# Performance work log

Hardware: AMD Instinct MI355X
Metric: run time of the kernel (lower is better)

## Reference

```python
import jax, jax.numpy as jnp
import numpy as np

B, T, C, H = 4, 2048, 1024, 16
D = C // H  # head dim = 64


def setup_inputs() -> dict:
    key = jax.random.key(0)
    k_x, k_wa, k_ba, k_wp, k_bp = jax.random.split(key, 5)
    s = 1.0 / np.sqrt(C)
    return {
        "x": jax.random.normal(k_x, (B, T, C), dtype=jnp.float32),
        "w_attn": jax.random.uniform(k_wa, (C, 3 * C), minval=-s, maxval=s, dtype=jnp.float32),
        "b_attn": jax.random.uniform(k_ba, (3 * C,), minval=-s, maxval=s, dtype=jnp.float32),
        "w_proj": jax.random.uniform(k_wp, (C, C), minval=-s, maxval=s, dtype=jnp.float32),
        "b_proj": jax.random.uniform(k_bp, (C,), minval=-s, maxval=s, dtype=jnp.float32),
    }


def reference(x, w_attn, b_attn, w_proj, b_proj):
    b, t, c = x.shape
    qkv = x @ w_attn + b_attn  # [b, t, 3c]
    q, k, v = jnp.split(qkv, 3, axis=-1)
    # [b, h, t, d]
    q = q.reshape(b, t, H, D).transpose(0, 2, 1, 3)
    k = k.reshape(b, t, H, D).transpose(0, 2, 1, 3)
    v = v.reshape(b, t, H, D).transpose(0, 2, 1, 3)
    scale = 1.0 / np.sqrt(D)
    logits = jnp.einsum("bhqd,bhkd->bhqk", q, k) * scale
    causal = jnp.tril(jnp.ones((t, t), dtype=bool))
    logits = jnp.where(causal, logits, jnp.finfo(logits.dtype).min)
    attn = jax.nn.softmax(logits, axis=-1)
    y = jnp.einsum("bhqk,bhkd->bhqd", attn, v)
    y = y.transpose(0, 2, 1, 3).reshape(b, t, c)
    return y @ w_proj + b_proj
```

## Files before the change

### kernel.cpp

```cpp
#include <hip/hip_runtime.h>


using u16 = unsigned short;
using u32 = unsigned int;
using bf16x8 = __attribute__((ext_vector_type(8))) __bf16;
using f32x4  = __attribute__((ext_vector_type(4))) float;
using f32x16 = __attribute__((ext_vector_type(16))) float;
using u16x8  = __attribute__((ext_vector_type(8))) u16;
using u16x4  = __attribute__((ext_vector_type(4))) u16;
using u32x2  = __attribute__((ext_vector_type(2))) u32;
using u32x4  = __attribute__((ext_vector_type(4))) u32;
using fvec4  = __attribute__((ext_vector_type(4))) float;

__device__ __forceinline__ u16 f2bf(float f) {
  u32 u = __builtin_bit_cast(u32, f);
  u32 r = (u + 0x7FFFu + ((u >> 16) & 1u)) >> 16;
  return (u16)r;
}

__device__ __forceinline__ u32 cvtpk(float lo, float hi) {
  u32 r;
  asm("v_cvt_pk_bf16_f32 %0, %1, %2" : "=v"(r) : "v"(lo), "v"(hi));
  return r;
}

__device__ __forceinline__ f32x4 mfma16(bf16x8 a, bf16x8 b, f32x4 c) {
  return __builtin_amdgcn_mfma_f32_16x16x32_bf16(a, b, c, 0, 0, 0);
}

__device__ __forceinline__ f32x16 mfma32(bf16x8 a, bf16x8 b, f32x16 c) {
  return __builtin_amdgcn_mfma_f32_32x32x16_bf16(a, b, c, 0, 0, 0);
}

__device__ __forceinline__ void gld16(const u16* g, u16* l) {
  __builtin_amdgcn_global_load_lds(
      (const __attribute__((address_space(1))) void*)g,
      (__attribute__((address_space(3))) void*)l, 16, 0, 0);
}

__global__ __launch_bounds__(256) void conv_kernel(
    const float* __restrict__ in, u16* __restrict__ out) {
  const size_t i = ((size_t)blockIdx.x * 256 + threadIdx.x) * 8;
  fvec4 a = *(const fvec4*)(in + i);
  fvec4 b = *(const fvec4*)(in + i + 4);
  u16x8 h;
#pragma unroll
  for (int j = 0; j < 4; ++j) { h[j] = f2bf(a[j]); h[4 + j] = f2bf(b[j]); }
  *(u16x8*)(out + i) = h;
}

__global__ __launch_bounds__(256) void transpose_conv_kernel(
    const float* __restrict__ W, u16* __restrict__ Wt, int K, int N) {
  __shared__ float tile[32][33];
  const int n0 = blockIdx.x * 32, k0 = blockIdx.y * 32;
  const int tx = threadIdx.x, ty = threadIdx.y;
#pragma unroll
  for (int j = 0; j < 4; ++j)
    tile[ty + j * 8][tx] = W[(size_t)(k0 + ty + j * 8) * N + n0 + tx];
  __syncthreads();
#pragma unroll
  for (int j = 0; j < 4; ++j)
    Wt[(size_t)(n0 + ty + j * 8) * K + k0 + tx] = f2bf(tile[tx][ty + j * 8]);
}

template <bool QKV>
__global__ __launch_bounds__(256) void gemm_kernel(
    const u16* __restrict__ A, const u16* __restrict__ Bt,
    const float* __restrict__ bias, void* __restrict__ Cp,
    u16* __restrict__ vt, int M, int N, int K) {
  constexpr float SC = 0.18033688011112042f;
  __shared__ u16 As[2][4096];
  __shared__ u16 Bs[2][4096];
  const int tid = threadIdx.x;
  const int l = tid & 63, w = tid >> 6;
  const int l15 = l & 15, l16 = l >> 4;
  const int wm = (w >> 1) * 64, wn = (w & 1) * 64;

  const u32 nwg = gridDim.x * gridDim.y;
  u32 f = blockIdx.y * gridDim.x + blockIdx.x;
  f = (f & 7) * (nwg >> 3) + (f >> 3);
  const long mbase = (long)(f / gridDim.x) * 128;
  const long nbase = (long)(f % gridDim.x) * 128;

  const int srow = tid >> 2;
  const int scol = ((tid & 3) ^ ((srow >> 1) & 3)) * 8;
  const u16* gA0 = A + (mbase + srow) * (long)K + scol;
  const u16* gA1 = gA0 + 64 * (long)K;
  const u16* gB0 = Bt + (nbase + srow) * (long)K + scol;
  const u16* gB1 = gB0 + 64 * (long)K;

  f32x4 acc[4][4] = {};
  const int NT = K >> 5;

#define STAGE(buf, koff)                         \
  gld16(gA0 + (koff), &As[buf][tid * 8]);        \
  gld16(gA1 + (koff), &As[buf][tid * 8 + 2048]); \
  gld16(gB0 + (koff), &Bs[buf][tid * 8]);        \
  gld16(gB1 + (koff), &Bs[buf][tid * 8 + 2048]);

  STAGE(0, 0);
  asm volatile("s_waitcnt vmcnt(0)" ::: "memory");
  __builtin_amdgcn_s_barrier();

  for (int t = 0; t < NT; ++t) {
    const int cur = t & 1;
    if (t + 1 < NT) { STAGE(cur ^ 1, (t + 1) * 32); }

    bf16x8 af[4], bfr[4];
#pragma unroll
    for (int i = 0; i < 4; ++i) {
      const int row = wm + i * 16 + l15;
      af[i] = *(const bf16x8*)(&As[cur][row * 32 + ((l16 ^ ((row >> 1) & 3)) * 8)]);
    }
#pragma unroll
    for (int j = 0; j < 4; ++j) {
      const int row = wn + j * 16 + l15;
      bfr[j] = *(const bf16x8*)(&Bs[cur][row * 32 + ((l16 ^ ((row >> 1) & 3)) * 8)]);
    }
    asm volatile("s_waitcnt lgkmcnt(0)" ::: "memory");
    __builtin_amdgcn_sched_barrier(0);
    __builtin_amdgcn_s_setprio(1);
#pragma unroll
    for (int i = 0; i < 4; ++i)
#pragma unroll
      for (int j = 0; j < 4; ++j)
        acc[i][j] = mfma16(af[i], bfr[j], acc[i][j]);
    __builtin_amdgcn_s_setprio(0);
    __builtin_amdgcn_sched_barrier(0);
    if (t + 1 < NT) { asm volatile("s_waitcnt vmcnt(0)" ::: "memory"); }
    __builtin_amdgcn_s_barrier();
  }
#undef STAGE

  if constexpr (QKV) {
    const bool isv = (nbase >= 2048);
#pragma unroll
    for (int i = 0; i < 4; ++i) {
#pragma unroll
      for (int j = 0; j < 4; ++j) {
        const long m0 = mbase + wm + i * 16 + l16 * 4;
        const int n = (int)nbase + wn + j * 16 + l15;
        const float bv = bias[n];
        if (!isv) {
          u16* qkp = (u16*)Cp;
          const float sc = (n < 1024) ? SC : 1.0f;
#pragma unroll
          for (int r = 0; r < 4; ++r)
            qkp[(m0 + r) * 2048 + n] = f2bf((acc[i][j][r] + bv) * sc);
        } else {
          const int vc = n - 2048, hh = vc >> 6, dd = vc & 63;
          const int bb = (int)(m0 >> 11), t0 = (int)(m0 & 2047);
          u16x4 pk;
#pragma unroll
          for (int r = 0; r < 4; ++r) pk[r] = f2bf(acc[i][j][r] + bv);
          *(u16x4*)(vt + ((size_t)(bb * 16 + hh) * 64 + dd) * 2048 + t0) = pk;
        }
      }
    }
  } else {
#pragma unroll
    for (int i = 0; i < 4; ++i) {
#pragma unroll
      for (int j = 0; j < 4; ++j) {
        const long row0 = mbase + wm + i * 16 + l16 * 4;
        const long col = nbase + wn + j * 16 + l15;
        const float bv = bias[col];
#pragma unroll
        for (int r = 0; r < 4; ++r)
          ((float*)Cp)[(row0 + r) * (long)N + col] = acc[i][j][r] + bv;
      }
    }
  }
}

__global__ __launch_bounds__(256, 2) void flash_kernel(
    const u16* __restrict__ qk, const u16* __restrict__ vt, u16* __restrict__ attn_out) {
  __shared__ u16 Ks[2][64 * 64];
  const int tid = threadIdx.x;
  const int lane = tid & 63, w = tid >> 6;
  const int l31 = lane & 31, hi = lane >> 5;
  const int xorv = (l31 & 7) << 4;

  const u32 i = blockIdx.y * 8 + blockIdx.x;
  const int jj = i >> 3;
  const int bh = (i & 7) | ((jj & 7) << 3);
  const int pair = (int)(i >> 6);
  const int b = bh >> 4, h = bh & 15;
  const u16* qbase = qk + (size_t)b * 2048 * 2048 + h * 64;
  const u16* kbase = qbase + 1024;
  const u16* vbase = vt + (size_t)bh * 64 * 2048;
  u16* obase = attn_out + (size_t)b * 2048 * 1024 + h * 64;

  const int srow = tid >> 3;
  const int sslot = (tid & 7) ^ (srow & 7);
  const u16* gk = kbase + (size_t)srow * 2048 + sslot * 8;

  int cur = 0;
  for (int half = 0; half < 2; ++half) {
    const int qt = half ? (15 - pair) : pair;
    const int nt = 2 * qt + 2;
    const int qr0 = qt * 128 + w * 32;
    const int q = qr0 + l31;

    bf16x8 qf[4];
#pragma unroll
    for (int ds = 0; ds < 4; ++ds)
      qf[ds] = *(const bf16x8*)(qbase + (size_t)q * 2048 + ds * 16 + hi * 8);

    f32x16 oacc[2] = {};
    float lsum = 0.f;

    gld16(gk, &Ks[cur][tid * 8]);
    gld16(gk + (size_t)32 * 2048, &Ks[cur][tid * 8 + 2048]);
    asm volatile("s_waitcnt vmcnt(0)" ::: "memory");
    __builtin_amdgcn_s_barrier();

    for (int kt = 0; kt < nt; ++kt) {
      const int kb = kt * 64;
      if (kt + 1 < nt) {
        gld16(gk + (size_t)(kb + 64) * 2048, &Ks[cur ^ 1][tid * 8]);
        gld16(gk + (size_t)(kb + 96) * 2048, &Ks[cur ^ 1][tid * 8 + 2048]);
      }
      u16x8 vf[2][4];
#pragma unroll
      for (int dh = 0; dh < 2; ++dh)
#pragma unroll
        for (int ks = 0; ks < 4; ++ks)
          vf[dh][ks] = *(const u16x8*)(vbase + (size_t)(dh * 32 + l31) * 2048 + kb + ks * 16 + hi * 8);

      f32x16 s0 = {}, s1 = {};
      __builtin_amdgcn_s_setprio(1);
#pragma unroll
      for (int ds = 0; ds < 4; ++ds) {
        const int col = (ds * 32 + hi * 16) ^ xorv;
        bf16x8 k0 = *(const bf16x8*)((const char*)&Ks[cur][0] + l31 * 128 + col);
        bf16x8 k1 = *(const bf16x8*)((const char*)&Ks[cur][0] + (32 + l31) * 128 + col);
        s0 = mfma32(k0, qf[ds], s0);
        s1 = mfma32(k1, qf[ds], s1);
      }
      __builtin_amdgcn_s_setprio(0);

      if (kb + 63 > qr0) {
#pragma unroll
        for (int r = 0; r < 16; ++r) {
          const int crow = (r & 3) + 8 * (r >> 2) + 4 * hi;
          if (kb + crow > q) s0[r] = -1e30f;
          if (kb + 32 + crow > q) s1[r] = -1e30f;
        }
      }

      float p0[16], p1[16];
      float ps = 0.f;
#pragma unroll
      for (int r = 0; r < 16; ++r) {
        p0[r] = exp2f(s0[r]);
        p1[r] = exp2f(s1[r]);
        ps += p0[r] + p1[r];
      }
      lsum += ps;

      bf16x8 pf[4];
#pragma unroll
      for (int kh = 0; kh < 2; ++kh) {
#pragma unroll
        for (int c = 0; c < 2; ++c) {
          const float* pp = kh ? p1 : p0;
          const int bs = c * 8;
          u32 L0 = cvtpk(pp[bs + 0], pp[bs + 1]);
          u32 L1 = cvtpk(pp[bs + 2], pp[bs + 3]);
          u32 L2 = cvtpk(pp[bs + 4], pp[bs + 5]);
          u32 L3 = cvtpk(pp[bs + 6], pp[bs + 7]);
          asm("v_permlane32_swap_b32 %0, %1" : "+v"(L0), "+v"(L2));
          asm("v_permlane32_swap_b32 %0, %1" : "+v"(L1), "+v"(L3));
          u32x4 pk = {L0, L1, L2, L3};
          pf[kh * 2 + c] = __builtin_bit_cast(bf16x8, pk);
        }
      }

      __builtin_amdgcn_s_setprio(1);
#pragma unroll
      for (int dh = 0; dh < 2; ++dh)
#pragma unroll
        for (int ks = 0; ks < 4; ++ks)
          oacc[dh] = mfma32(__builtin_bit_cast(bf16x8, vf[dh][ks]), pf[ks], oacc[dh]);
      __builtin_amdgcn_s_setprio(0);

      asm volatile("s_waitcnt vmcnt(0)" ::: "memory");
      __builtin_amdgcn_s_barrier();
      cur ^= 1;
    }

    lsum += __shfl_xor(lsum, 32);
    const float inv = 1.0f / lsum;
    u16* orow = obase + (size_t)q * 1024;
#pragma unroll
    for (int dh = 0; dh < 2; ++dh) {
#pragma unroll
      for (int jq = 0; jq < 4; ++jq) {
        u32x2 pk;
        pk[0] = cvtpk(oacc[dh][jq * 4 + 0] * inv, oacc[dh][jq * 4 + 1] * inv);
        pk[1] = cvtpk(oacc[dh][jq * 4 + 2] * inv, oacc[dh][jq * 4 + 3] * inv);
        *(u32x2*)(orow + dh * 32 + 8 * jq + 4 * hi) = pk;
      }
    }
  }
}

extern "C" void kernel_launch(void* const* d_in, const int* in_sizes, int n_in,
                              void* d_out, int out_size, void* d_ws, size_t ws_size,
                              hipStream_t stream) {
  (void)in_sizes; (void)n_in; (void)out_size; (void)ws_size;
  const float* x      = (const float*)d_in[0];
  const float* w_attn = (const float*)d_in[1];
  const float* b_attn = (const float*)d_in[2];
  const float* w_proj = (const float*)d_in[3];
  const float* b_proj = (const float*)d_in[4];
  float* out = (float*)d_out;

  char* ws = (char*)d_ws;
  u16* qkbuf = (u16*)(ws);
  u16* vtbuf = (u16*)(ws + 33554432);
  u16* xbf   = (u16*)(ws + 50331648);
  u16* attnb = (u16*)(ws + 50331648);
  u16* wtA   = (u16*)(ws + 67108864);
  u16* wtP   = (u16*)(ws + 73400320);

  conv_kernel<<<4096, 256, 0, stream>>>(x, xbf);
  transpose_conv_kernel<<<dim3(3072 / 32, 1024 / 32), dim3(32, 8), 0, stream>>>(w_attn, wtA, 1024, 3072);
  transpose_conv_kernel<<<dim3(1024 / 32, 1024 / 32), dim3(32, 8), 0, stream>>>(w_proj, wtP, 1024, 1024);

  gemm_kernel<true><<<dim3(3072 / 128, 8192 / 128), 256, 0, stream>>>(
      xbf, wtA, b_attn, qkbuf, vtbuf, 8192, 3072, 1024);

  flash_kernel<<<dim3(8, 64), 256, 0, stream>>>(qkbuf, vtbuf, attnb);

  gemm_kernel<false><<<dim3(1024 / 128, 8192 / 128), 256, 0, stream>>>(
      attnb, wtP, b_proj, out, nullptr, 8192, 1024, 1024);
}
```

Measured before the change: 203.4 us.

## Fuse x fp32-to-bf16 conversion into QKV GEMM and stage V in LDS

The separate conversion kernel for x is removed. The QKV GEMM now loads fp32 activations directly, converts them in registers and writes bf16 to LDS, which saves one kernel launch and a round trip of a bf16 copy through memory. Separately, the flash kernel moves to 128-key tiles and DMA-stages both K and V into swizzled LDS instead of reading V from global memory per lane. It also skips 32-key blocks that lie fully above the causal diagonal. Costs: the GEMM A path becomes register-staged instead of async DMA and reads twice the bytes, and the flash kernel's LDS use grows, which may reduce occupancy.

```diff
diff --git a/kernel.cpp b/kernel.cpp
--- a/kernel.cpp
+++ b/kernel.cpp
@@ -38,17 +38,6 @@
       (__attribute__((address_space(3))) void*)l, 16, 0, 0);
 }
 
-__global__ __launch_bounds__(256) void conv_kernel(
-    const float* __restrict__ in, u16* __restrict__ out) {
-  const size_t i = ((size_t)blockIdx.x * 256 + threadIdx.x) * 8;
-  fvec4 a = *(const fvec4*)(in + i);
-  fvec4 b = *(const fvec4*)(in + i + 4);
-  u16x8 h;
-#pragma unroll
-  for (int j = 0; j < 4; ++j) { h[j] = f2bf(a[j]); h[4 + j] = f2bf(b[j]); }
-  *(u16x8*)(out + i) = h;
-}
-
 __global__ __launch_bounds__(256) void transpose_conv_kernel(
     const float* __restrict__ W, u16* __restrict__ Wt, int K, int N) {
   __shared__ float tile[32][33];
@@ -63,9 +52,9 @@
     Wt[(size_t)(n0 + ty + j * 8) * K + k0 + tx] = f2bf(tile[tx][ty + j * 8]);
 }
 
-template <bool QKV>
+template <bool AF32, bool QKV>
 __global__ __launch_bounds__(256) void gemm_kernel(
-    const u16* __restrict__ A, const u16* __restrict__ Bt,
+    const void* __restrict__ Ap, const u16* __restrict__ Bt,
     const float* __restrict__ bias, void* __restrict__ Cp,
     u16* __restrict__ vt, int M, int N, int K) {
   constexpr float SC = 0.18033688011112042f;
@@ -83,28 +72,66 @@
   const long nbase = (long)(f % gridDim.x) * 128;
 
   const int srow = tid >> 2;
-  const int scol = ((tid & 3) ^ ((srow >> 1) & 3)) * 8;
-  const u16* gA0 = A + (mbase + srow) * (long)K + scol;
-  const u16* gA1 = gA0 + 64 * (long)K;
-  const u16* gB0 = Bt + (nbase + srow) * (long)K + scol;
+  const int ck = tid & 3;
+  const int slotA = (ck ^ ((srow >> 1) & 3)) * 8;
+  const u16* gB0 = Bt + (nbase + srow) * (long)K + slotA;
   const u16* gB1 = gB0 + 64 * (long)K;
+  const u16* gA0u = nullptr; const u16* gA1u = nullptr;
+  const float* gA0f = nullptr; const float* gA1f = nullptr;
+  if constexpr (AF32) {
+    gA0f = (const float*)Ap + (mbase + srow) * (long)K + ck * 8;
+    gA1f = gA0f + 64 * (long)K;
+  } else {
+    gA0u = (const u16*)Ap + (mbase + srow) * (long)K + slotA;
+    gA1u = gA0u + 64 * (long)K;
+  }
 
   f32x4 acc[4][4] = {};
   const int NT = K >> 5;
 
-#define STAGE(buf, koff)                         \
-  gld16(gA0 + (koff), &As[buf][tid * 8]);        \
-  gld16(gA1 + (koff), &As[buf][tid * 8 + 2048]); \
+#define STAGE_B(buf, koff)                       \
   gld16(gB0 + (koff), &Bs[buf][tid * 8]);        \
   gld16(gB1 + (koff), &Bs[buf][tid * 8 + 2048]);
 
-  STAGE(0, 0);
-  asm volatile("s_waitcnt vmcnt(0)" ::: "memory");
+#define STAGE_A_DMA(buf, koff)                   \
+  gld16(gA0u + (koff), &As[buf][tid * 8]);       \
+  gld16(gA1u + (koff), &As[buf][tid * 8 + 2048]);
+
+  STAGE_B(0, 0);
+  if constexpr (AF32) {
+    fvec4 a0 = *(const fvec4*)(gA0f);
+    fvec4 a1 = *(const fvec4*)(gA0f + 4);
+    fvec4 a2 = *(const fvec4*)(gA1f);
+    fvec4 a3 = *(const fvec4*)(gA1f + 4);
+    u16x8 h0, h1;
+#pragma unroll
+    for (int j = 0; j < 4; ++j) {
+      h0[j] = f2bf(a0[j]); h0[4 + j] = f2bf(a1[j]);
+      h1[j] = f2bf(a2[j]); h1[4 + j] = f2bf(a3[j]);
+    }
+    *(u16x8*)(&As[0][srow * 32 + slotA]) = h0;
+    *(u16x8*)(&As[0][(srow + 64) * 32 + slotA]) = h1;
+  } else {
+    STAGE_A_DMA(0, 0);
+  }
+  asm volatile("s_waitcnt vmcnt(0) lgkmcnt(0)" ::: "memory");
   __builtin_amdgcn_s_barrier();
 
   for (int t = 0; t < NT; ++t) {
     const int cur = t & 1;
-    if (t + 1 < NT) { STAGE(cur ^ 1, (t + 1) * 32); }
+    fvec4 a0, a1, a2, a3;
+    if (t + 1 < NT) {
+      STAGE_B(cur ^ 1, (t + 1) * 32);
+      if constexpr (AF32) {
+        const int kn = (t + 1) * 32;
+        a0 = *(const fvec4*)(gA0f + kn);
+        a1 = *(const fvec4*)(gA0f + kn + 4);
+        a2 = *(const fvec4*)(gA1f + kn);
+        a3 = *(const fvec4*)(gA1f + kn + 4);
+      } else {
+        STAGE_A_DMA(cur ^ 1, (t + 1) * 32);
+      }
+    }
 
     bf16x8 af[4], bfr[4];
 #pragma unroll
@@ -127,10 +154,24 @@
         acc[i][j] = mfma16(af[i], bfr[j], acc[i][j]);
     __builtin_amdgcn_s_setprio(0);
     __builtin_amdgcn_sched_barrier(0);
-    if (t + 1 < NT) { asm volatile("s_waitcnt vmcnt(0)" ::: "memory"); }
+
+    if (t + 1 < NT) {
+      if constexpr (AF32) {
+        u16x8 h0, h1;
+#pragma unroll
+        for (int j = 0; j < 4; ++j) {
+          h0[j] = f2bf(a0[j]); h0[4 + j] = f2bf(a1[j]);
+          h1[j] = f2bf(a2[j]); h1[4 + j] = f2bf(a3[j]);
+        }
+        *(u16x8*)(&As[cur ^ 1][srow * 32 + slotA]) = h0;
+        *(u16x8*)(&As[cur ^ 1][(srow + 64) * 32 + slotA]) = h1;
+      }
+      asm volatile("s_waitcnt vmcnt(0) lgkmcnt(0)" ::: "memory");
+    }
     __builtin_amdgcn_s_barrier();
   }
-#undef STAGE
+#undef STAGE_B
+#undef STAGE_A_DMA
 
   if constexpr (QKV) {
     const bool isv = (nbase >= 2048);
@@ -175,11 +216,13 @@
 
 __global__ __launch_bounds__(256, 2) void flash_kernel(
     const u16* __restrict__ qk, const u16* __restrict__ vt, u16* __restrict__ attn_out) {
-  __shared__ u16 Ks[2][64 * 64];
+  __shared__ u16 Ks[2][128 * 64];
+  __shared__ u16 Vs[2][64 * 128];
   const int tid = threadIdx.x;
   const int lane = tid & 63, w = tid >> 6;
   const int l31 = lane & 31, hi = lane >> 5;
-  const int xorv = (l31 & 7) << 4;
+  const int xorK = (l31 & 7) << 4;
+  const int xorV = (l31 & 15) << 4;
 
   const u32 i = blockIdx.y * 8 + blockIdx.x;
   const int jj = i >> 3;
@@ -191,16 +234,24 @@
   const u16* vbase = vt + (size_t)bh * 64 * 2048;
   u16* obase = attn_out + (size_t)b * 2048 * 1024 + h * 64;
 
-  const int srow = tid >> 3;
-  const int sslot = (tid & 7) ^ (srow & 7);
-  const u16* gk = kbase + (size_t)srow * 2048 + sslot * 8;
+  const int kslot = ((tid & 7) ^ ((tid >> 3) & 7)) * 8;
+  const int vslot = ((tid & 15) ^ ((tid >> 4) & 15)) * 8;
+  const u16* gk = kbase + (size_t)(tid >> 3) * 2048 + kslot;
+  const u16* gv = vbase + (size_t)(tid >> 4) * 2048 + vslot;
+
+#define DMA_TILE(buf, kb_)                                              \
+  _Pragma("unroll") for (int p_ = 0; p_ < 4; ++p_) {                    \
+    gld16(gk + (size_t)((kb_) + p_ * 32) * 2048, &Ks[buf][tid * 8 + p_ * 2048]); \
+    gld16(gv + (size_t)(p_ * 16) * 2048 + (kb_), &Vs[buf][tid * 8 + p_ * 2048]); \
+  }
 
   int cur = 0;
   for (int half = 0; half < 2; ++half) {
     const int qt = half ? (15 - pair) : pair;
-    const int nt = 2 * qt + 2;
+    const int nt = qt + 1;
     const int qr0 = qt * 128 + w * 32;
     const int q = qr0 + l31;
+    const int qmax = qr0 + 31;
 
     bf16x8 qf[4];
 #pragma unroll
@@ -210,79 +261,68 @@
     f32x16 oacc[2] = {};
     float lsum = 0.f;
 
-    gld16(gk, &Ks[cur][tid * 8]);
-    gld16(gk + (size_t)32 * 2048, &Ks[cur][tid * 8 + 2048]);
+    DMA_TILE(cur, 0);
     asm volatile("s_waitcnt vmcnt(0)" ::: "memory");
     __builtin_amdgcn_s_barrier();
 
     for (int kt = 0; kt < nt; ++kt) {
-      const int kb = kt * 64;
-      if (kt + 1 < nt) {
-        gld16(gk + (size_t)(kb + 64) * 2048, &Ks[cur ^ 1][tid * 8]);
-        gld16(gk + (size_t)(kb + 96) * 2048, &Ks[cur ^ 1][tid * 8 + 2048]);
-      }
-      u16x8 vf[2][4];
+      const int kb = kt * 128;
+      if (kt + 1 < nt) { DMA_TILE(cur ^ 1, kb + 128); }
+
+      bf16x8 pf[8];
+#pragma unroll
+      for (int kblk = 0; kblk < 4; ++kblk) {
+        const int kb32 = kb + kblk * 32;
+        if (kb32 <= qmax) {
+          f32x16 s = {};
+          __builtin_amdgcn_s_setprio(1);
+#pragma unroll
+          for (int ds = 0; ds < 4; ++ds) {
+            bf16x8 kf = *(const bf16x8*)((const char*)&Ks[cur][0] +
+                          (kblk * 32 + l31) * 128 + ((ds * 32 + hi * 16) ^ xorK));
+            s = mfma32(kf, qf[ds], s);
+          }
+          __builtin_amdgcn_s_setprio(0);
+
+          if (kb32 + 31 > qr0) {
+#pragma unroll
+            for (int r = 0; r < 16; ++r) {
+              const int key = kb32 + (r & 3) + 8 * (r >> 2) + 4 * hi;
+              if (key > q) s[r] = -1e30f;
+            }
+          }
+
+          float ps = 0.f;
+#pragma unroll
+          for (int r = 0; r < 16; ++r) { s[r] = exp2f(s[r]); ps += s[r]; }
+          lsum += ps;
+
+#pragma unroll
+          for (int c = 0; c < 2; ++c) {
+            const int bs = c * 8;
+            u32 L0 = cvtpk(s[bs + 0], s[bs + 1]);
+            u32 L1 = cvtpk(s[bs + 2], s[bs + 3]);
+            u32 L2 = cvtpk(s[bs + 4], s[bs + 5]);
+            u32 L3 = cvtpk(s[bs + 6], s[bs + 7]);
+            asm("v_permlane32_swap_b32 %0, %1" : "+v"(L0), "+v"(L2));
+            asm("v_permlane32_swap_b32 %0, %1" : "+v"(L1), "+v"(L3));
+            u32x4 pk = {L0, L1, L2, L3};
+            pf[kblk * 2 + c] = __builtin_bit_cast(bf16x8, pk);
+          }
+        }
+      }
+
+      __builtin_amdgcn_s_setprio(1);
 #pragma unroll
       for (int dh = 0; dh < 2; ++dh)
 #pragma unroll
-        for (int ks = 0; ks < 4; ++ks)
-          vf[dh][ks] = *(const u16x8*)(vbase + (size_t)(dh * 32 + l31) * 2048 + kb + ks * 16 + hi * 8);
-
-      f32x16 s0 = {}, s1 = {};
-      __builtin_amdgcn_s_setprio(1);
-#pragma unroll
-      for (int ds = 0; ds < 4; ++ds) {
-        const int col = (ds * 32 + hi * 16) ^ xorv;
-        bf16x8 k0 = *(const bf16x8*)((const char*)&Ks[cur][0] + l31 * 128 + col);
-        bf16x8 k1 = *(const bf16x8*)((const char*)&Ks[cur][0] + (32 + l31) * 128 + col);
-        s0 = mfma32(k0, qf[ds], s0);
-        s1 = mfma32(k1, qf[ds], s1);
-      }
-      __builtin_amdgcn_s_setprio(0);
-
-      if (kb + 63 > qr0) {
-#pragma unroll
-        for (int r = 0; r < 16; ++r) {
-          const int crow = (r & 3) + 8 * (r >> 2) + 4 * hi;
-          if (kb + crow > q) s0[r] = -1e30f;
-          if (kb + 32 + crow > q) s1[r] = -1e30f;
+        for (int ks = 0; ks < 8; ++ks) {
+          if (kb + (ks >> 1) * 32 <= qmax) {
+            bf16x8 vf = *(const bf16x8*)((const char*)&Vs[cur][0] +
+                          (dh * 32 + l31) * 256 + ((ks * 32 + hi * 16) ^ xorV));
+            oacc[dh] = mfma32(vf, pf[ks], oacc[dh]);
+          }
         }
-      }
-
-      float p0[16], p1[16];
-      float ps = 0.f;
-#pragma unroll
-      for (int r = 0; r < 16; ++r) {
-        p0[r] = exp2f(s0[r]);
-        p1[r] = exp2f(s1[r]);
-        ps += p0[r] + p1[r];
-      }
-      lsum += ps;
-
-      bf16x8 pf[4];
-#pragma unroll
-      for (int kh = 0; kh < 2; ++kh) {
-#pragma unroll
-        for (int c = 0; c < 2; ++c) {
-          const float* pp = kh ? p1 : p0;
-          const int bs = c * 8;
-          u32 L0 = cvtpk(pp[bs + 0], pp[bs + 1]);
-          u32 L1 = cvtpk(pp[bs + 2], pp[bs + 3]);
-          u32 L2 = cvtpk(pp[bs + 4], pp[bs + 5]);
-          u32 L3 = cvtpk(pp[bs + 6], pp[bs + 7]);
-          asm("v_permlane32_swap_b32 %0, %1" : "+v"(L0), "+v"(L2));
-          asm("v_permlane32_swap_b32 %0, %1" : "+v"(L1), "+v"(L3));
-          u32x4 pk = {L0, L1, L2, L3};
-          pf[kh * 2 + c] = __builtin_bit_cast(bf16x8, pk);
-        }
-      }
-
-      __builtin_amdgcn_s_setprio(1);
-#pragma unroll
-      for (int dh = 0; dh < 2; ++dh)
-#pragma unroll
-        for (int ks = 0; ks < 4; ++ks)
-          oacc[dh] = mfma32(__builtin_bit_cast(bf16x8, vf[dh][ks]), pf[ks], oacc[dh]);
       __builtin_amdgcn_s_setprio(0);
 
       asm volatile("s_waitcnt vmcnt(0)" ::: "memory");
@@ -304,6 +344,7 @@
       }
     }
   }
+#undef DMA_TILE
 }
 
 extern "C" void kernel_launch(void* const* d_in, const int* in_sizes, int n_in,
@@ -320,20 +361,18 @@
   char* ws = (char*)d_ws;
   u16* qkbuf = (u16*)(ws);
   u16* vtbuf = (u16*)(ws + 33554432);
-  u16* xbf   = (u16*)(ws + 50331648);
   u16* attnb = (u16*)(ws + 50331648);
   u16* wtA   = (u16*)(ws + 67108864);
   u16* wtP   = (u16*)(ws + 73400320);
 
-  conv_kernel<<<4096, 256, 0, stream>>>(x, xbf);
   transpose_conv_kernel<<<dim3(3072 / 32, 1024 / 32), dim3(32, 8), 0, stream>>>(w_attn, wtA, 1024, 3072);
   transpose_conv_kernel<<<dim3(1024 / 32, 1024 / 32), dim3(32, 8), 0, stream>>>(w_proj, wtP, 1024, 1024);
 
-  gemm_kernel<true><<<dim3(3072 / 128, 8192 / 128), 256, 0, stream>>>(
-      xbf, wtA, b_attn, qkbuf, vtbuf, 8192, 3072, 1024);
+  gemm_kernel<true, true><<<dim3(3072 / 128, 8192 / 128), 256, 0, stream>>>(
+      x, wtA, b_attn, qkbuf, vtbuf, 8192, 3072, 1024);
 
   flash_kernel<<<dim3(8, 64), 256, 0, stream>>>(qkbuf, vtbuf, attnb);
 
-  gemm_kernel<false><<<dim3(1024 / 128, 8192 / 128), 256, 0, stream>>>(
+  gemm_kernel<false, false><<<dim3(1024 / 128, 8192 / 128), 256, 0, stream>>>(
       attnb, wtP, b_proj, out, nullptr, 8192, 1024, 1024);
 }
```

Result: faster. 185.9 us (-8.6%).
